# Kernel optimization log

Measured on AMD Instinct MI355X. Metric: run time of the kernel, lower is better.

The kernel has to match this reference:

```python
import jax, jax.numpy as jnp
import numpy as np

EPS = 1e-5

def conv3x3(x, w, b=None):
    # NCHW, OIHW, stride 1, padding 1
    y = jax.lax.conv_general_dilated(x, w, (1, 1), ((1, 1), (1, 1)),
                                     dimension_numbers=('NCHW', 'OIHW', 'NCHW'))
    if b is not None:
        y = y + b[None, :, None, None]
    return y

def batchnorm(x, g, b):
    # training-mode BN (PyTorch default): biased variance over (N,H,W)
    m = x.mean((0, 2, 3), keepdims=True)
    v = x.var((0, 2, 3), keepdims=True)
    return (x - m) * jax.lax.rsqrt(v + EPS) * g[None, :, None, None] + b[None, :, None, None]

def upsample2x_align_corners(x):
    # bilinear, align_corners=True, scale_factor=2
    def lerp_axis(a, Lin, axis):
        Lout = 2 * Lin
        c = jnp.arange(Lout, dtype=a.dtype) * (Lin - 1) / (Lout - 1)
        i0 = jnp.floor(c).astype(jnp.int32)
        i1 = jnp.minimum(i0 + 1, Lin - 1)
        w = c - i0.astype(a.dtype)
        shape = [1] * a.ndim
        shape[axis] = Lout
        w = w.reshape(shape)
        return jnp.take(a, i0, axis=axis) * (1 - w) + jnp.take(a, i1, axis=axis) * w
    x = lerp_axis(x, x.shape[2], 2)
    x = lerp_axis(x, x.shape[3], 3)
    return x

def deform_sample(x, offsets):
    # torchvision DeformConv2d v1 sampling: kernel 3x3, pad 1, offsets [B,18,H,W]
    # layout: per kernel point k (row-major), channels (2k, 2k+1) = (dy, dx)
    B, C, H, W = x.shape
    K = 9
    off = offsets.reshape(B, K, 2, H, W)
    ky, kx = jnp.meshgrid(jnp.arange(3) - 1, jnp.arange(3) - 1, indexing='ij')
    ky = ky.reshape(K).astype(x.dtype)
    kx = kx.reshape(K).astype(x.dtype)
    gy = jnp.arange(H, dtype=x.dtype)[None, None, :, None]
    gx = jnp.arange(W, dtype=x.dtype)[None, None, None, :]
    py = gy + ky[None, :, None, None] + off[:, :, 0]  # [B,K,H,W]
    px = gx + kx[None, :, None, None] + off[:, :, 1]
    y0 = jnp.floor(py)
    x0 = jnp.floor(px)
    wy = (py - y0)[:, None]  # [B,1,K,H,W]
    wx = (px - x0)[:, None]
    y0i = y0.astype(jnp.int32)
    x0i = x0.astype(jnp.int32)
    x_flat = x.reshape(B, C, H * W)
    def gather(yi, xi):
        valid = ((yi >= 0) & (yi < H) & (xi >= 0) & (xi < W))
        idx = jnp.clip(yi, 0, H - 1) * W + jnp.clip(xi, 0, W - 1)  # [B,K,H,W]
        g = jnp.take_along_axis(x_flat, idx.reshape(B, 1, K * H * W), axis=2)
        return g.reshape(B, C, K, H, W) * valid[:, None].astype(x.dtype)
    v00 = gather(y0i, x0i)
    v01 = gather(y0i, x0i + 1)
    v10 = gather(y0i + 1, x0i)
    v11 = gather(y0i + 1, x0i + 1)
    return (v00 * (1 - wy) * (1 - wx) + v01 * (1 - wy) * wx
            + v10 * wy * (1 - wx) + v11 * wy * wx)

def setup_inputs() -> dict:
    key = jax.random.key(0)
    ks = jax.random.split(key, 6)
    B, in_ch, skip_ch, out_ch = 4, 256, 128, 128
    Hs, Ws = 128, 128
    x = jax.random.normal(ks[0], (B, in_ch, Hs // 2, Ws // 2), jnp.float32)
    skip = jax.random.normal(ks[1], (B, skip_ch, Hs, Ws), jnp.float32)
    cat_ch = in_ch + skip_ch
    conv1_w = jax.random.normal(ks[2], (out_ch, cat_ch, 3, 3), jnp.float32) * (2.0 / (cat_ch * 9)) ** 0.5
    off_w = jax.random.normal(ks[3], (18, out_ch, 3, 3), jnp.float32) * 0.01
    off_b = jnp.zeros((18,), jnp.float32)
    def_w = jax.random.normal(ks[4], (out_ch, out_ch, 3, 3), jnp.float32) * (2.0 / (out_ch * 9)) ** 0.5
    def_b = jnp.zeros((out_ch,), jnp.float32)
    return {
        'x': x, 'skip': skip,
        'conv1_w': conv1_w,
        'bn1_g': jnp.ones((out_ch,), jnp.float32), 'bn1_b': jnp.zeros((out_ch,), jnp.float32),
        'off_w': off_w, 'off_b': off_b,
        'def_w': def_w, 'def_b': def_b,
        'bn2_g': jnp.ones((out_ch,), jnp.float32), 'bn2_b': jnp.zeros((out_ch,), jnp.float32),
    }

def reference(x, skip, conv1_w, bn1_g, bn1_b, off_w, off_b, def_w, def_b, bn2_g, bn2_b):
    xu = upsample2x_align_corners(x)
    dh = skip.shape[2] - xu.shape[2]
    dw = skip.shape[3] - xu.shape[3]
    if dh != 0 or dw != 0:
        xu = jnp.pad(xu, ((0, 0), (0, 0), (dh // 2, dh - dh // 2), (dw // 2, dw - dw // 2)))
    cat = jnp.concatenate([skip, xu], axis=1)
    h = jax.nn.relu(batchnorm(conv3x3(cat, conv1_w), bn1_g, bn1_b))
    offsets = conv3x3(h, off_w, off_b)  # [B,18,H,W]
    sampled = deform_sample(h, offsets)  # [B,C,9,H,W]
    O = def_w.shape[0]
    y = jnp.einsum('ock,bckhw->bohw', def_w.reshape(O, def_w.shape[1], 9), sampled)
    y = y + def_b[None, :, None, None]
    return jax.nn.relu(batchnorm(y, bn2_g, bn2_b))
```

## Files before the change

kernel.cpp:

```cpp
#include <hip/hip_runtime.h>
#include <hip/hip_bf16.h>

typedef __hip_bfloat16 bf16;
typedef __bf16 bf16x8 __attribute__((ext_vector_type(8)));
typedef __bf16 bf16x4 __attribute__((ext_vector_type(4)));
typedef float  f32x4  __attribute__((ext_vector_type(4)));

constexpr int NB   = 4;
constexpr int H    = 128;
constexpr int W    = 128;
constexpr int HW   = H * W;
constexpr int NPIX = NB * HW;
constexpr int CCAT = 384;
constexpr int CSKIP= 128;
constexpr int CIN  = 256;
constexpr int CO   = 128;
constexpr int HS   = 64;
constexpr int WP   = 130;
constexpr int K1   = 3456;
constexpr int KD   = 1152;
constexpr int NBORD= 2 * WP + 2 * (WP - 2);
constexpr float EPS = 1e-5f;

__device__ __forceinline__ float b2f(bf16 v){ return __bfloat162float(v); }
__device__ __forceinline__ bf16  f2b(float v){ return __float2bfloat16(v); }

__device__ __forceinline__ void async_copy16(const void* g, void* s){
    __builtin_amdgcn_global_load_lds((const __attribute__((address_space(1))) void*)g,
                                     (__attribute__((address_space(3))) void*)s, 16, 0, 0);
}

__device__ __forceinline__ void border_yx(int p, int& y, int& x){
    if (p < WP)             { y = 0;        x = p; }
    else if (p < 2 * WP)    { y = WP - 1;   x = p - WP; }
    else if (p < 2 * WP + (WP - 2)) { y = p - 2 * WP + 1;          x = 0; }
    else                    { y = p - (2 * WP + (WP - 2)) + 1;     x = WP - 1; }
}

__global__ void k_prep(float* __restrict__ sums, bf16* __restrict__ catp,
                       bf16* __restrict__ hp){
    int i = blockIdx.x * blockDim.x + threadIdx.x;
    int stride = gridDim.x * blockDim.x;
    for (int j = i; j < 512; j += stride) sums[j] = 0.f;
    const int nCat = NB * NBORD * CCAT;
    for (int j = i; j < nCat; j += stride){
        int c = j % CCAT, r = j / CCAT, p = r % NBORD, b = r / NBORD;
        int y, x; border_yx(p, y, x);
        catp[(((size_t)b * WP + y) * WP + x) * CCAT + c] = f2b(0.f);
    }
    const int nHp = NB * NBORD * CO;
    for (int j = i; j < nHp; j += stride){
        int c = j % CO, r = j / CO, p = r % NBORD, b = r / NBORD;
        int y, x; border_yx(p, y, x);
        hp[(((size_t)b * WP + y) * WP + x) * CO + c] = f2b(0.f);
    }
}

__global__ __launch_bounds__(256) void k_build_cat2(const float* __restrict__ x,
                                                    const float* __restrict__ skip,
                                                    bf16* __restrict__ catp){
    constexpr int TS = 66;
    __shared__ bf16 tile[128 * TS];
    int t  = threadIdx.x;
    int y  = blockIdx.x % H, b = blockIdx.x / H;
    int xx = t & 127, cp = t >> 7;

    float cy = (y * 63.0f) / 127.0f;
    int   y0 = (int)cy;
    int   y1 = min(y0 + 1, HS - 1);
    float wy = cy - y0;
    float cxf = (xx * 63.0f) / 127.0f;
    int   x0 = (int)cxf;
    int   x1 = min(x0 + 1, HS - 1);
    float wx = cxf - x0;

    bf16* orow = catp + (((size_t)b * WP + y + 1) * WP + 1) * CCAT;

    for (int chunk = 0; chunk < 6; chunk++){
        int cbase = chunk * 64;
        if (chunk >= 1) __syncthreads();
        if (chunk < 2){
            const float* sb = skip + ((size_t)(b * CSKIP + cbase + cp * 32) * H + y) * W;
#pragma unroll
            for (int i = 0; i < 32; i++)
                tile[xx * TS + cp * 32 + i] = f2b(sb[(size_t)i * HW + xx]);
        } else {
            int icb = (chunk - 2) * 64 + cp * 32;
            const float* xr0 = x + ((size_t)(b * CIN + icb) * HS + y0) * HS;
            const float* xr1 = x + ((size_t)(b * CIN + icb) * HS + y1) * HS;
#pragma unroll
            for (int i = 0; i < 32; i++){
                const float* r0 = xr0 + (size_t)i * HS * HS;
                const float* r1 = xr1 + (size_t)i * HS * HS;
                float v0 = r0[x0] * (1 - wx) + r0[x1] * wx;
                float v1 = r1[x0] * (1 - wx) + r1[x1] * wx;
                tile[xx * TS + cp * 32 + i] = f2b(v0 * (1 - wy) + v1 * wy);
            }
        }
        __syncthreads();
        int cc2 = (t & 31) * 2;
        int px0 = t >> 5;
#pragma unroll
        for (int pp = 0; pp < 16; pp++){
            int px = pp * 8 + px0;
            unsigned int v = *(const unsigned int*)&tile[px * TS + cc2];
            *(unsigned int*)&orow[(size_t)px * CCAT + cbase + cc2] = v;
        }
    }
}

__global__ void k_tr_all(const float* __restrict__ w1, const float* __restrict__ wo,
                         const float* __restrict__ wd,
                         bf16* __restrict__ wt1, bf16* __restrict__ wto,
                         bf16* __restrict__ wtd){
    int i = blockIdx.x * blockDim.x + threadIdx.x;
    if (i < CO * K1){
        int e  = i & 7;
        int l  = (i >> 3) & 63;
        int nb = (i >> 9) & 7;
        int ks = (i >> 12) & 1;
        int p  = i >> 13;
        int gp = p / 6, q = p - gp * 6;
        int ky = gp / 3, ci = gp - ky * 3;
        int kx = q >> 1, s64 = q & 1;
        int oc = nb * 16 + (l & 15);
        int ic = ci * 128 + s64 * 64 + ks * 32 + (l >> 4) * 8 + e;
        wt1[i] = f2b(w1[((oc * CCAT + ic) * 3 + ky) * 3 + kx]);
        return;
    }
    i -= CO * K1;
    if (i < 32 * KD){
        int kk = i % KD, o = i / KD;
        int ky = kk / 384, r = kk % 384, kx = r >> 7, ic = r & 127;
        wto[i] = (o < 18) ? f2b(wo[((o * CO + ic) * 3 + ky) * 3 + kx]) : f2b(0.f);
        return;
    }
    i -= 32 * KD;
    if (i < CO * KD){
        int kk = i % KD, o = i / KD;
        int kp = kk >> 7, c = kk & 127;
        wtd[i] = f2b(wd[(o * CO + c) * 9 + kp]);
    }
}

__global__ __launch_bounds__(256) void k_conv1_mfma(const bf16* __restrict__ catp,
                                                    const bf16* __restrict__ wbt,
                                                    bf16* __restrict__ hp,
                                                    float* __restrict__ sums){
    __shared__ unsigned short Ab[2][68 * 128];
    __shared__ float ps[256];
    int t = threadIdx.x;
    int l = t & 63, w = t >> 6;
    int half = blockIdx.x & 1;
    int y = (blockIdx.x >> 1) % H, b = blockIdx.x / (2 * H);
    int px0 = half * 64;

    int m = l & 15, quad = l >> 4;

    f32x4 acc[4][2];
#pragma unroll
    for (int i = 0; i < 4; i++)
#pragma unroll
        for (int j = 0; j < 2; j++) acc[i][j] = f32x4{0.f, 0.f, 0.f, 0.f};

    const size_t rowStride = (size_t)WP * CCAT;
    const char* wq = (const char*)wbt + w * 2048 + l * 16;

    bf16x8 bA[2][2], bB[2][2];

    {
        const bf16* Arow = catp + ((size_t)(b * WP) + y) * rowStride + (size_t)px0 * CCAT;
        for (int i = w; i < 17; i += 4){
            int G = i * 64 + l;
            int px = G >> 4, ol = G & 15;
            int osrc = ol ^ (px & 7);
            async_copy16(Arow + (size_t)px * CCAT + osrc * 8, &Ab[0][i * 512]);
        }
#pragma unroll
        for (int ks = 0; ks < 2; ks++)
#pragma unroll
            for (int ni = 0; ni < 2; ni++)
                bA[ks][ni] = *(const bf16x8*)(wq + ks * 8192 + ni * 1024);
    }
    __syncthreads();

#pragma unroll 1
    for (int g = 0; g < 9; g++){
        if (g < 8){
            int gn = g + 1;
            int kyn = gn / 3, cin = gn - kyn * 3;
            const bf16* Arow = catp + ((size_t)(b * WP) + y + kyn) * rowStride
                             + (size_t)px0 * CCAT + cin * 128;
            for (int i = w; i < 17; i += 4){
                int G = i * 64 + l;
                int px = G >> 4, ol = G & 15;
                int osrc = ol ^ (px & 7);
                async_copy16(Arow + (size_t)px * CCAT + osrc * 8, &Ab[gn & 1][i * 512]);
            }
        }
        const bf16x8* ap = (const bf16x8*)&Ab[g & 1][0];
        const char* wg = wq + (size_t)g * 6 * 16384;
#pragma unroll
        for (int j = 0; j < 6; j++){
            int kx = j >> 1, s64 = j & 1;
            const char* wnx = wg + (j + 1) * 16384;
            if (j & 1){
#pragma unroll
                for (int ks = 0; ks < 2; ks++)
#pragma unroll
                    for (int ni = 0; ni < 2; ni++)
                        bA[ks][ni] = *(const bf16x8*)(wnx + ks * 8192 + ni * 1024);
            } else {
#pragma unroll
                for (int ks = 0; ks < 2; ks++)
#pragma unroll
                    for (int ni = 0; ni < 2; ni++)
                        bB[ks][ni] = *(const bf16x8*)(wnx + ks * 8192 + ni * 1024);
            }
#pragma unroll
            for (int ks = 0; ks < 2; ks++){
                int s = s64 * 2 + ks;
                bf16x8 af[4];
#pragma unroll
                for (int mi = 0; mi < 4; mi++){
                    int pxk = mi * 16 + m + kx;
                    af[mi] = ap[pxk * 16 + ((s * 4 + quad) ^ (pxk & 7))];
                }
                if (j & 1){
#pragma unroll
                    for (int mi = 0; mi < 4; mi++)
#pragma unroll
                        for (int ni = 0; ni < 2; ni++)
                            acc[mi][ni] = __builtin_amdgcn_mfma_f32_16x16x32_bf16(
                                af[mi], bB[ks][ni], acc[mi][ni], 0, 0, 0);
                } else {
#pragma unroll
                    for (int mi = 0; mi < 4; mi++)
#pragma unroll
                        for (int ni = 0; ni < 2; ni++)
                            acc[mi][ni] = __builtin_amdgcn_mfma_f32_16x16x32_bf16(
                                af[mi], bA[ks][ni], acc[mi][ni], 0, 0, 0);
                }
            }
        }
        __syncthreads();
    }

    size_t obase = (((size_t)b * WP + y + 1) * WP + 1 + px0) * CO;
#pragma unroll
    for (int mi = 0; mi < 4; mi++){
        int p0 = mi * 16 + quad * 4;
#pragma unroll
        for (int ni = 0; ni < 2; ni++){
            int oc = w * 32 + ni * 16 + m;
#pragma unroll
            for (int r = 0; r < 4; r++)
                hp[obase + (size_t)(p0 + r) * CO + oc] = f2b(acc[mi][ni][r]);
        }
    }
    ps[t] = 0.f;
    __syncthreads();
#pragma unroll
    for (int ni = 0; ni < 2; ni++){
        int ch = w * 32 + ni * 16 + m;
        float s = 0.f, q2 = 0.f;
#pragma unroll
        for (int mi = 0; mi < 4; mi++)
#pragma unroll
            for (int r = 0; r < 4; r++){
                float v = acc[mi][ni][r];
                s += v; q2 += v * v;
            }
        s += __shfl_xor(s, 16); s += __shfl_xor(s, 32);
        q2 += __shfl_xor(q2, 16); q2 += __shfl_xor(q2, 32);
        if (quad == 0){
            atomicAdd(&ps[ch], s);
            atomicAdd(&ps[128 + ch], q2);
        }
    }
    __syncthreads();
    if (t < 128){
        atomicAdd(&sums[t],       ps[t]);
        atomicAdd(&sums[128 + t], ps[128 + t]);
    }
}

__global__ __launch_bounds__(256) void k_bn_apply_pad(bf16* __restrict__ t,
                                                      const float* __restrict__ sums,
                                                      const float* __restrict__ g,
                                                      const float* __restrict__ bb){
    __shared__ float ssc[256];
    int tt = threadIdx.x;
    if (tt < 128){
        float mean = sums[tt] / (float)NPIX;
        float var  = sums[128 + tt] / (float)NPIX - mean * mean;
        float scale = g[tt] * rsqrtf(var + EPS);
        ssc[tt]       = scale;
        ssc[128 + tt] = bb[tt] - mean * scale;
    }
    __syncthreads();
    int i = blockIdx.x * 256 + tt;
    if (i >= NPIX * CO) return;
    int c = i & 127;
    int pix = i >> 7;
    int xw = pix & 127, yh = (pix >> 7) & 127, b = pix >> 14;
    size_t a = (((size_t)b * WP + yh + 1) * WP + xw + 1) * CO + c;
    float v = b2f(t[a]) * ssc[c] + ssc[128 + c];
    t[a] = f2b(v > 0.f ? v : 0.f);
}

__global__ __launch_bounds__(256) void k_conv_off_mfma(const bf16* __restrict__ hp,
                                                       const bf16* __restrict__ wob,
                                                       const float* __restrict__ off_b,
                                                       bf16* __restrict__ offs){
    __shared__ unsigned short Ab[132 * 128];
    __shared__ unsigned short Bb[32 * 384];
    int t = threadIdx.x, l = t & 63, w = t >> 6;
    int y = blockIdx.x % H, b = blockIdx.x / H;
    int m = l & 15, quad = l >> 4;
    int wm = w & 1, wn = w >> 1;

    f32x4 acc[4];
#pragma unroll
    for (int i = 0; i < 4; i++) acc[i] = f32x4{0.f, 0.f, 0.f, 0.f};

    const size_t rowStrideH = (size_t)WP * CO;
    for (int ky = 0; ky < 3; ky++){
        const bf16* Arow = hp + ((size_t)(b * WP) + y + ky) * rowStrideH;
        __syncthreads();
        for (int i = w; i < 33; i += 4){
            int G  = i * 64 + l;
            int px = G >> 4, ol = G & 15;
            int osrc = ol ^ (px & 7);
            async_copy16(Arow + (size_t)px * CO + osrc * 8, &Ab[i * 512]);
        }
        for (int i = w; i < 24; i += 4){
            int g  = i * 64 + l;
            int kx = g >> 9, oc = (g >> 4) & 31, ol = g & 15;
            int osrc = ol ^ (oc & 7);
            async_copy16(wob + (size_t)oc * KD + ky * 384 + kx * 128 + osrc * 8,
                         &Bb[i * 512]);
        }
        __syncthreads();
        const bf16x8* ap = (const bf16x8*)Ab;
        const bf16x8* bp = (const bf16x8*)Bb;
        for (int kx = 0; kx < 3; kx++){
#pragma unroll
            for (int s = 0; s < 4; s++){
                int oc = wn * 16 + m;
                bf16x8 bfr = bp[kx * 512 + oc * 16 + ((s * 4 + quad) ^ (oc & 7))];
#pragma unroll
                for (int mi = 0; mi < 4; mi++){
                    int pxk = wm * 64 + mi * 16 + m + kx;
                    bf16x8 af = ap[pxk * 16 + ((s * 4 + quad) ^ (pxk & 7))];
                    acc[mi] = __builtin_amdgcn_mfma_f32_16x16x32_bf16(af, bfr, acc[mi], 0, 0, 0);
                }
            }
        }
    }
    int oc = wn * 16 + m;
    if (oc < 18){
        float bias = off_b[oc];
        int rowpix = b * HW + y * W;
#pragma unroll
        for (int mi = 0; mi < 4; mi++){
            int p0 = wm * 64 + mi * 16 + quad * 4;
#pragma unroll
            for (int r = 0; r < 4; r++)
                offs[(size_t)(rowpix + p0 + r) * 18 + oc] = f2b(acc[mi][r] + bias);
        }
    }
}

__global__ __launch_bounds__(256) void k_deform_mfma(const bf16* __restrict__ hp,
                                                     const bf16* __restrict__ offs,
                                                     const bf16* __restrict__ wdb,
                                                     const float* __restrict__ def_b,
                                                     bf16* __restrict__ y,
                                                     float* __restrict__ sums){
    __shared__ unsigned short Ab[128 * 64];
    __shared__ unsigned short Bb[128 * 64];
    __shared__ int2   sc_yx[9 * 128];
    __shared__ float4 sc_w[9 * 128];
    __shared__ float  ps[256];

    int t = threadIdx.x, l = t & 63, w = t >> 6;
    int yrow = blockIdx.x % H, b = blockIdx.x / H;
    int rowpix = b * HW + yrow * W;

    for (int idx = t; idx < 9 * 128; idx += 256){
        int kp = idx >> 7, px = idx & 127;
        float dy = b2f(offs[(size_t)(rowpix + px) * 18 + 2 * kp]);
        float dx = b2f(offs[(size_t)(rowpix + px) * 18 + 2 * kp + 1]);
        float py = yrow + (kp / 3 - 1) + dy;
        float pxx = px + (kp % 3 - 1) + dx;
        float fy = floorf(py), fx = floorf(pxx);
        float wy = py - fy, wx = pxx - fx;
        int y0 = (int)fy, x0 = (int)fx;
        bool vy0 = (y0 >= 0) && (y0 < H);
        bool vy1 = (y0 + 1 >= 0) && (y0 + 1 < H);
        bool vx0 = (x0 >= 0) && (x0 < W);
        bool vx1 = (x0 + 1 >= 0) && (x0 + 1 < W);
        int y0c = min(max(y0, 0), H - 1),     y1c = min(max(y0 + 1, 0), H - 1);
        int x0c = min(max(x0, 0), W - 1),     x1c = min(max(x0 + 1, 0), W - 1);
        sc_yx[idx] = make_int2(((y0c + 1) * WP) | (((y1c + 1) * WP) << 16),
                               (x0c + 1) | ((x1c + 1) << 16));
        sc_w[idx] = make_float4((1 - wy) * (1 - wx) * (float)(vy0 && vx0),
                                (1 - wy) * wx       * (float)(vy0 && vx1),
                                wy * (1 - wx)       * (float)(vy1 && vx0),
                                wy * wx             * (float)(vy1 && vx1));
    }
    __syncthreads();

    int pr = l >> 3, koct = (l & 7) ^ pr;
    int m = l & 15, quad = l >> 4;
    int wm = w & 1, wn = w >> 1;
    int g = l >> 4, j = l & 15;

    f32x4 acc[4][4];
#pragma unroll
    for (int i = 0; i < 4; i++)
#pragma unroll
        for (int jj = 0; jj < 4; jj++) acc[i][jj] = f32x4{0.f, 0.f, 0.f, 0.f};

    const bf16* hpb = hp + (size_t)b * WP * WP * CO;

    for (int kc = 0; kc < 18; kc++){
        int kp = kc >> 1, ch = (kc & 1) * 64;
        __syncthreads();
        int kg = kp * 128 + ch;
#pragma unroll
        for (int i = 0; i < 4; i++){
            int oc = w * 32 + i * 8 + pr;
            async_copy16(wdb + (size_t)oc * KD + kg + koct * 8,
                         &Bb[(w * 32 + i * 8) * 64]);
        }
        int cb = ch + j * 4;
#pragma unroll
        for (int p = 0; p < 8; p++){
            int px = w * 32 + g * 8 + p;
            int idx = kp * 128 + px;
            int2 yx = sc_yx[idx];
            float4 w4 = sc_w[idx];
            int r0 = yx.x & 0xffff, r1 = ((unsigned)yx.x) >> 16;
            int c0 = yx.y & 0xffff, c1 = ((unsigned)yx.y) >> 16;
            const bf16* base = hpb + cb;
            bf16x4 s00 = *(const bf16x4*)(base + (size_t)(r0 + c0) * CO);
            bf16x4 s01 = *(const bf16x4*)(base + (size_t)(r0 + c1) * CO);
            bf16x4 s10 = *(const bf16x4*)(base + (size_t)(r1 + c0) * CO);
            bf16x4 s11 = *(const bf16x4*)(base + (size_t)(r1 + c1) * CO);
            bf16x4 pv;
#pragma unroll
            for (int r = 0; r < 4; r++){
                float v = w4.x * (float)s00[r] + w4.y * (float)s01[r]
                        + w4.z * (float)s10[r] + w4.w * (float)s11[r];
                pv[r] = (__bf16)v;
            }
            int oct_sw = (j >> 1) ^ (px & 7);
            *(bf16x4*)&Ab[px * 64 + oct_sw * 8 + (j & 1) * 4] = pv;
        }
        __syncthreads();
        const bf16x8* ap = (const bf16x8*)Ab;
        const bf16x8* bp = (const bf16x8*)Bb;
#pragma unroll
        for (int ks = 0; ks < 2; ks++){
            bf16x8 af[4], bfr[4];
#pragma unroll
            for (int mi = 0; mi < 4; mi++){
                int px = wm * 64 + mi * 16 + m;
                af[mi] = ap[px * 8 + ((ks * 4 + quad) ^ (px & 7))];
            }
#pragma unroll
            for (int ni = 0; ni < 4; ni++){
                int oc = wn * 64 + ni * 16 + m;
                bfr[ni] = bp[oc * 8 + ((ks * 4 + quad) ^ (oc & 7))];
            }
#pragma unroll
            for (int mi = 0; mi < 4; mi++)
#pragma unroll
                for (int ni = 0; ni < 4; ni++)
                    acc[mi][ni] = __builtin_amdgcn_mfma_f32_16x16x32_bf16(
                        af[mi], bfr[ni], acc[mi][ni], 0, 0, 0);
        }
    }
#pragma unroll
    for (int mi = 0; mi < 4; mi++){
        int p0 = wm * 64 + mi * 16 + quad * 4;
#pragma unroll
        for (int ni = 0; ni < 4; ni++){
            int oc = wn * 64 + ni * 16 + m;
            float bias = def_b[oc];
#pragma unroll
            for (int r = 0; r < 4; r++)
                y[(size_t)(rowpix + p0 + r) * CO + oc] = f2b(acc[mi][ni][r] + bias);
        }
    }
    ps[t] = 0.f;
    __syncthreads();
#pragma unroll
    for (int ni = 0; ni < 4; ni++){
        int ch = wn * 64 + ni * 16 + m;
        float bias = def_b[ch];
        float s = 0.f, q = 0.f;
#pragma unroll
        for (int mi = 0; mi < 4; mi++)
#pragma unroll
            for (int r = 0; r < 4; r++){
                float v = acc[mi][ni][r] + bias;
                s += v; q += v * v;
            }
        s += __shfl_xor(s, 16); s += __shfl_xor(s, 32);
        q += __shfl_xor(q, 16); q += __shfl_xor(q, 32);
        if (quad == 0){
            atomicAdd(&ps[ch], s);
            atomicAdd(&ps[128 + ch], q);
        }
    }
    __syncthreads();
    if (t < 128){
        atomicAdd(&sums[t],       ps[t]);
        atomicAdd(&sums[128 + t], ps[128 + t]);
    }
}

__global__ __launch_bounds__(256) void k_final(const bf16* __restrict__ yb,
                                               const float* __restrict__ sums,
                                               const float* __restrict__ g,
                                               const float* __restrict__ bb,
                                               float* __restrict__ out){
    __shared__ unsigned short tile[128 * 129];
    __shared__ float ssc[256];
    int t = threadIdx.x;
    if (t < 128){
        float mean = sums[t] / (float)NPIX;
        float var  = sums[128 + t] / (float)NPIX - mean * mean;
        float scale = g[t] * rsqrtf(var + EPS);
        ssc[t]       = scale;
        ssc[128 + t] = bb[t] - mean * scale;
    }
    int yrow = blockIdx.x % H, b = blockIdx.x / H;
    int rowbase = b * HW + yrow * W;
    const unsigned short* src = (const unsigned short*)yb;
    for (int it = 0; it < 64; it++){
        int idx = it * 256 + t;
        int c = idx & 127, px = idx >> 7;
        tile[px * 129 + c] = src[(size_t)(rowbase + px) * CO + c];
    }
    __syncthreads();
    for (int it = 0; it < 64; it++){
        int idx = it * 256 + t;
        int xw = idx & 127, o = idx >> 7;
        unsigned short u = tile[xw * 129 + o];
        float v = (float)(*(const __bf16*)&u);
        v = v * ssc[o] + ssc[128 + o];
        out[(((size_t)b * CO + o) * H + yrow) * W + xw] = v > 0.f ? v : 0.f;
    }
}

extern "C" void kernel_launch(void* const* d_in, const int* in_sizes, int n_in,
                              void* d_out, int out_size, void* d_ws, size_t ws_size,
                              hipStream_t stream){
    const float* x      = (const float*)d_in[0];
    const float* skip   = (const float*)d_in[1];
    const float* conv1w = (const float*)d_in[2];
    const float* bn1g   = (const float*)d_in[3];
    const float* bn1b   = (const float*)d_in[4];
    const float* offw   = (const float*)d_in[5];
    const float* offb   = (const float*)d_in[6];
    const float* defw   = (const float*)d_in[7];
    const float* defb   = (const float*)d_in[8];
    const float* bn2g   = (const float*)d_in[9];
    const float* bn2b   = (const float*)d_in[10];
    float* out = (float*)d_out;

    char* ws = (char*)d_ws;
    size_t off_bytes = 0;
    auto alloc = [&](size_t bytes) -> void* {
        void* p = ws + off_bytes;
        off_bytes += (bytes + 255) & ~(size_t)255;
        return p;
    };
    const size_t catp_elems = (size_t)NB * WP * WP * CCAT;
    const size_t hp_elems   = (size_t)NB * WP * WP * CO;
    bf16*  catp  = (bf16*) alloc(catp_elems * 2 + 2048);
    bf16*  hp    = (bf16*) alloc(hp_elems * 2);
    bf16*  offs  = (bf16*) alloc((size_t)NPIX * 18 * 2);
    bf16*  yb    = (bf16*) alloc((size_t)NPIX * CO * 2);
    bf16*  wbt   = (bf16*) alloc((size_t)CO * K1 * 2 + 32768);
    bf16*  wob   = (bf16*) alloc((size_t)32 * KD * 2);
    bf16*  wdb   = (bf16*) alloc((size_t)CO * KD * 2);
    float* sums  = (float*)alloc(512 * 4);
    float* sums1 = sums;
    float* sums2 = sums + 256;

    k_prep<<<1024, 256, 0, stream>>>(sums, catp, hp);

    k_build_cat2<<<NB * H, 256, 0, stream>>>(x, skip, catp);

    const int ntr = CO * K1 + 32 * KD + CO * KD;
    k_tr_all<<<(ntr + 255) / 256, 256, 0, stream>>>(conv1w, offw, defw, wbt, wob, wdb);

    k_conv1_mfma<<<NB * H * 2, 256, 0, stream>>>(catp, wbt, hp, sums1);

    k_bn_apply_pad<<<(NPIX * CO + 255) / 256, 256, 0, stream>>>(hp, sums1, bn1g, bn1b);

    k_conv_off_mfma<<<NB * H, 256, 0, stream>>>(hp, wob, offb, offs);

    k_deform_mfma<<<NB * H, 256, 0, stream>>>(hp, offs, wdb, defb, yb, sums2);

    k_final<<<NB * H, 256, 0, stream>>>(yb, sums2, bn2g, bn2b, out);
}
```

Before: 333.9 us.

## Pre-swizzle offset/deform weights into MFMA fragment order and double-buffer deform sampling

```diff
diff --git a/kernel.cpp b/kernel.cpp
--- a/kernel.cpp
+++ b/kernel.cpp
@@ -130,16 +130,29 @@
     }
     i -= CO * K1;
     if (i < 32 * KD){
-        int kk = i % KD, o = i / KD;
-        int ky = kk / 384, r = kk % 384, kx = r >> 7, ic = r & 127;
-        wto[i] = (o < 18) ? f2b(wo[((o * CO + ic) * 3 + ky) * 3 + kx]) : f2b(0.f);
+        int e  = i & 7;
+        int l  = (i >> 3) & 63;
+        int wn = (i >> 9) & 1;
+        int s  = (i >> 10) & 3;
+        int kk = i >> 12;
+        int ky = kk / 3, kx = kk - ky * 3;
+        int oc = wn * 16 + (l & 15);
+        int ic = s * 32 + (l >> 4) * 8 + e;
+        wto[i] = (oc < 18) ? f2b(wo[((oc * CO + ic) * 3 + ky) * 3 + kx]) : f2b(0.f);
         return;
     }
     i -= 32 * KD;
     if (i < CO * KD){
-        int kk = i % KD, o = i / KD;
-        int kp = kk >> 7, c = kk & 127;
-        wtd[i] = f2b(wd[(o * CO + c) * 9 + kp]);
+        int e  = i & 7;
+        int l  = (i >> 3) & 63;
+        int ni = (i >> 9) & 3;
+        int wn = (i >> 11) & 1;
+        int ks = (i >> 12) & 1;
+        int kc = i >> 13;
+        int oc = wn * 64 + ni * 16 + (l & 15);
+        int ic = (kc & 1) * 64 + ks * 32 + (l >> 4) * 8 + e;
+        int kp = kc >> 1;
+        wtd[i] = f2b(wd[(oc * CO + ic) * 9 + kp]);
     }
 }
 
@@ -313,47 +326,47 @@
                                                        const bf16* __restrict__ wob,
                                                        const float* __restrict__ off_b,
                                                        bf16* __restrict__ offs){
-    __shared__ unsigned short Ab[132 * 128];
-    __shared__ unsigned short Bb[32 * 384];
+    __shared__ unsigned short Ab[68 * 128];
     int t = threadIdx.x, l = t & 63, w = t >> 6;
-    int y = blockIdx.x % H, b = blockIdx.x / H;
+    int half = blockIdx.x & 1;
+    int y = (blockIdx.x >> 1) % H, b = blockIdx.x / (2 * H);
+    int px0 = half * 64;
     int m = l & 15, quad = l >> 4;
     int wm = w & 1, wn = w >> 1;
 
-    f32x4 acc[4];
-#pragma unroll
-    for (int i = 0; i < 4; i++) acc[i] = f32x4{0.f, 0.f, 0.f, 0.f};
+    f32x4 acc[2];
+#pragma unroll
+    for (int i = 0; i < 2; i++) acc[i] = f32x4{0.f, 0.f, 0.f, 0.f};
 
     const size_t rowStrideH = (size_t)WP * CO;
+    const char* wq = (const char*)wob + wn * 1024 + l * 16;
+
     for (int ky = 0; ky < 3; ky++){
-        const bf16* Arow = hp + ((size_t)(b * WP) + y + ky) * rowStrideH;
-        __syncthreads();
-        for (int i = w; i < 33; i += 4){
+        if (ky) __syncthreads();
+        const bf16* Arow = hp + ((size_t)(b * WP) + y + ky) * rowStrideH
+                         + (size_t)px0 * CO;
+        for (int i = w; i < 17; i += 4){
             int G  = i * 64 + l;
             int px = G >> 4, ol = G & 15;
             int osrc = ol ^ (px & 7);
             async_copy16(Arow + (size_t)px * CO + osrc * 8, &Ab[i * 512]);
         }
-        for (int i = w; i < 24; i += 4){
-            int g  = i * 64 + l;
-            int kx = g >> 9, oc = (g >> 4) & 31, ol = g & 15;
-            int osrc = ol ^ (oc & 7);
-            async_copy16(wob + (size_t)oc * KD + ky * 384 + kx * 128 + osrc * 8,
-                         &Bb[i * 512]);
-        }
+        bf16x8 bfr[3][4];
+#pragma unroll
+        for (int kx = 0; kx < 3; kx++)
+#pragma unroll
+            for (int s = 0; s < 4; s++)
+                bfr[kx][s] = *(const bf16x8*)(wq + (((ky * 3 + kx) * 4 + s) * 2048));
         __syncthreads();
         const bf16x8* ap = (const bf16x8*)Ab;
-        const bf16x8* bp = (const bf16x8*)Bb;
         for (int kx = 0; kx < 3; kx++){
 #pragma unroll
             for (int s = 0; s < 4; s++){
-                int oc = wn * 16 + m;
-                bf16x8 bfr = bp[kx * 512 + oc * 16 + ((s * 4 + quad) ^ (oc & 7))];
-#pragma unroll
-                for (int mi = 0; mi < 4; mi++){
-                    int pxk = wm * 64 + mi * 16 + m + kx;
+#pragma unroll
+                for (int mi = 0; mi < 2; mi++){
+                    int pxk = wm * 32 + mi * 16 + m + kx;
                     bf16x8 af = ap[pxk * 16 + ((s * 4 + quad) ^ (pxk & 7))];
-                    acc[mi] = __builtin_amdgcn_mfma_f32_16x16x32_bf16(af, bfr, acc[mi], 0, 0, 0);
+                    acc[mi] = __builtin_amdgcn_mfma_f32_16x16x32_bf16(af, bfr[kx][s], acc[mi], 0, 0, 0);
                 }
             }
         }
@@ -361,10 +374,10 @@
     int oc = wn * 16 + m;
     if (oc < 18){
         float bias = off_b[oc];
-        int rowpix = b * HW + y * W;
-#pragma unroll
-        for (int mi = 0; mi < 4; mi++){
-            int p0 = wm * 64 + mi * 16 + quad * 4;
+        int rowpix = b * HW + y * W + px0;
+#pragma unroll
+        for (int mi = 0; mi < 2; mi++){
+            int p0 = wm * 32 + mi * 16 + quad * 4;
 #pragma unroll
             for (int r = 0; r < 4; r++)
                 offs[(size_t)(rowpix + p0 + r) * 18 + oc] = f2b(acc[mi][r] + bias);
@@ -378,8 +391,7 @@
                                                      const float* __restrict__ def_b,
                                                      bf16* __restrict__ y,
                                                      float* __restrict__ sums){
-    __shared__ unsigned short Ab[128 * 64];
-    __shared__ unsigned short Bb[128 * 64];
+    __shared__ unsigned short Ab[2][128 * 64];
     __shared__ int2   sc_yx[9 * 128];
     __shared__ float4 sc_w[9 * 128];
     __shared__ float  ps[256];
@@ -412,7 +424,6 @@
     }
     __syncthreads();
 
-    int pr = l >> 3, koct = (l & 7) ^ pr;
     int m = l & 15, quad = l >> 4;
     int wm = w & 1, wn = w >> 1;
     int g = l >> 4, j = l & 15;
@@ -424,17 +435,10 @@
         for (int jj = 0; jj < 4; jj++) acc[i][jj] = f32x4{0.f, 0.f, 0.f, 0.f};
 
     const bf16* hpb = hp + (size_t)b * WP * WP * CO;
-
-    for (int kc = 0; kc < 18; kc++){
+    const char* wq = (const char*)wdb + wn * 4096 + l * 16;
+
+    auto GEN = [&](int kc, unsigned short* dst){
         int kp = kc >> 1, ch = (kc & 1) * 64;
-        __syncthreads();
-        int kg = kp * 128 + ch;
-#pragma unroll
-        for (int i = 0; i < 4; i++){
-            int oc = w * 32 + i * 8 + pr;
-            async_copy16(wdb + (size_t)oc * KD + kg + koct * 8,
-                         &Bb[(w * 32 + i * 8) * 64]);
-        }
         int cb = ch + j * 4;
 #pragma unroll
         for (int p = 0; p < 8; p++){
@@ -457,30 +461,39 @@
                 pv[r] = (__bf16)v;
             }
             int oct_sw = (j >> 1) ^ (px & 7);
-            *(bf16x4*)&Ab[px * 64 + oct_sw * 8 + (j & 1) * 4] = pv;
-        }
+            *(bf16x4*)&dst[px * 64 + oct_sw * 8 + (j & 1) * 4] = pv;
+        }
+    };
+
+    GEN(0, &Ab[0][0]);
+
+#pragma unroll 1
+    for (int kc = 0; kc < 18; kc++){
         __syncthreads();
-        const bf16x8* ap = (const bf16x8*)Ab;
-        const bf16x8* bp = (const bf16x8*)Bb;
+        bf16x8 bfr[2][4];
+        const char* wk = wq + (size_t)kc * 16384;
+#pragma unroll
+        for (int ks = 0; ks < 2; ks++)
+#pragma unroll
+            for (int ni = 0; ni < 4; ni++)
+                bfr[ks][ni] = *(const bf16x8*)(wk + ks * 8192 + ni * 1024);
+        if (kc < 17) GEN(kc + 1, &Ab[(kc + 1) & 1][0]);
+
+        const bf16x8* ap = (const bf16x8*)&Ab[kc & 1][0];
 #pragma unroll
         for (int ks = 0; ks < 2; ks++){
-            bf16x8 af[4], bfr[4];
+            bf16x8 af[4];
 #pragma unroll
             for (int mi = 0; mi < 4; mi++){
                 int px = wm * 64 + mi * 16 + m;
                 af[mi] = ap[px * 8 + ((ks * 4 + quad) ^ (px & 7))];
             }
 #pragma unroll
-            for (int ni = 0; ni < 4; ni++){
-                int oc = wn * 64 + ni * 16 + m;
-                bfr[ni] = bp[oc * 8 + ((ks * 4 + quad) ^ (oc & 7))];
-            }
-#pragma unroll
             for (int mi = 0; mi < 4; mi++)
 #pragma unroll
                 for (int ni = 0; ni < 4; ni++)
                     acc[mi][ni] = __builtin_amdgcn_mfma_f32_16x16x32_bf16(
-                        af[mi], bfr[ni], acc[mi][ni], 0, 0, 0);
+                        af[mi], bfr[ks][ni], acc[mi][ni], 0, 0, 0);
         }
     }
 #pragma unroll
@@ -583,7 +596,7 @@
     const size_t catp_elems = (size_t)NB * WP * WP * CCAT;
     const size_t hp_elems   = (size_t)NB * WP * WP * CO;
     bf16*  catp  = (bf16*) alloc(catp_elems * 2 + 2048);
-    bf16*  hp    = (bf16*) alloc(hp_elems * 2);
+    bf16*  hp    = (bf16*) alloc(hp_elems * 2 + 2048);
     bf16*  offs  = (bf16*) alloc((size_t)NPIX * 18 * 2);
     bf16*  yb    = (bf16*) alloc((size_t)NPIX * CO * 2);
     bf16*  wbt   = (bf16*) alloc((size_t)CO * K1 * 2 + 32768);
@@ -604,7 +617,7 @@
 
     k_bn_apply_pad<<<(NPIX * CO + 255) / 256, 256, 0, stream>>>(hp, sums1, bn1g, bn1b);
 
-    k_conv_off_mfma<<<NB * H, 256, 0, stream>>>(hp, wob, offb, offs);
+    k_conv_off_mfma<<<NB * H * 2, 256, 0, stream>>>(hp, wob, offb, offs);
 
     k_deform_mfma<<<NB * H, 256, 0, stream>>>(hp, offs, wdb, defb, yb, sums2);
 
```

New measurement: 332.6 us. No clear change (-0.4%).
